# Performance work log

Hardware: AMD Instinct MI355X
Metric: run time of the kernel (lower is better)

Reference implementation:

```python
import jax, jax.numpy as jnp
import numpy as np

B, GS, IN_H, GCN_H, LIN_H = 65536, 7, 5, 144, 128


def _xavier(key, shape):
    fan_in, fan_out = shape[0], shape[1]
    limit = np.sqrt(6.0 / (fan_in + fan_out)).astype(np.float32)
    return jax.random.uniform(key, shape, jnp.float32, -limit, limit)


def setup_inputs() -> dict:
    key = jax.random.key(0)
    ks = jax.random.split(key, 12)
    operations = jax.random.normal(ks[0], (B, GS, IN_H), jnp.float32)
    adjacency = (jax.random.uniform(ks[1], (B, GS, GS)) < 0.3).astype(jnp.float32)
    num_vertices = jax.random.randint(ks[2], (B,), 1, 8).astype(jnp.float32)
    w1_0 = _xavier(ks[3], (IN_H, GCN_H))
    w2_0 = _xavier(ks[4], (IN_H, GCN_H))
    w1_1 = _xavier(ks[5], (GCN_H, GCN_H))
    w2_1 = _xavier(ks[6], (GCN_H, GCN_H))
    w1_2 = _xavier(ks[7], (GCN_H, GCN_H))
    w2_2 = _xavier(ks[8], (GCN_H, GCN_H))
    fc1_w = _xavier(ks[9], (LIN_H, GCN_H))  # torch Linear stores [out, in]
    fc2_w = _xavier(ks[10], (1, LIN_H))
    return {
        'operations': operations, 'adjacency': adjacency, 'num_vertices': num_vertices,
        'w1_0': w1_0, 'w2_0': w2_0, 'w1_1': w1_1, 'w2_1': w2_1,
        'w1_2': w1_2, 'w2_2': w2_2, 'fc1_w': fc1_w, 'fc2_w': fc2_w,
    }


def _row_normalize(adj):
    # divide each row by its sum (matches torch normalize_adj)
    return adj / adj.sum(axis=2, keepdims=True)


def reference(operations, adjacency, num_vertices,
              w1_0, w2_0, w1_1, w2_1, w1_2, w2_2, fc1_w, fc2_w):
    gs = adjacency.shape[1]
    eye = jnp.eye(gs, dtype=adjacency.dtype)
    adj_d = _row_normalize(adjacency + eye)  # [B, gs, gs]
    x = operations
    for w1, w2 in ((w1_0, w2_0), (w1_1, w2_1), (w1_2, w2_2)):
        norm_adj = _row_normalize(adj_d)                      # identity in value, kept faithful
        inv_norm_adj = _row_normalize(adj_d.transpose(0, 2, 1))
        o1 = jax.nn.relu(jnp.einsum('bij,bjk->bik', norm_adj, x @ w1))
        o2 = jax.nn.relu(jnp.einsum('bij,bjk->bik', inv_norm_adj, x @ w2))
        x = (o1 + o2) * 0.5  # dropout is identity at inference
    pooled = x.sum(axis=1) / num_vertices[:, None]            # [B, gcn_hidden]
    h = pooled @ fc1_w.T                                      # [B, linear_hidden]
    out = (h @ fc2_w.T).reshape(-1)                           # [B]
    return out
```

## Files before the change

### kernel.cpp

```cpp
#include <hip/hip_runtime.h>


typedef _Float16 half8   __attribute__((ext_vector_type(8)));
typedef _Float16 half4_t __attribute__((ext_vector_type(4)));
typedef float    floatx16 __attribute__((ext_vector_type(16)));

constexpr int GS = 7;
constexpr int NI = 4;
constexpr int MROWS = NI * GS;
constexpr int H = 144;
constexpr int LSTRIDE = 2 * 5 * 9 * 512;
constexpr int WT_HALFS = 3 * LSTRIDE;
constexpr int FRAGS = 3 * 90 * 64;
constexpr int XROW = 152;
constexpr int YROW = 40;

static __device__ inline half8 bc(_Float16 v) {
    half8 h = {v, v, v, v, v, v, v, v};
    return h;
}

__global__ void prep_kernel(const float* __restrict__ w10, const float* __restrict__ w20,
                            const float* __restrict__ w11, const float* __restrict__ w21,
                            const float* __restrict__ w12, const float* __restrict__ w22,
                            const float* __restrict__ fc1, const float* __restrict__ fc2,
                            _Float16* __restrict__ wt, float* __restrict__ g)
{
    if (blockIdx.x == 68) {
        const int j = threadIdx.x;
        if (j < H) {
            float s = 0.f;
            for (int o = 0; o < 128; ++o) s = fmaf(fc2[o], fc1[o * H + j], s);
            g[j] = s;
        }
        return;
    }
    const int t = blockIdx.x * 256 + threadIdx.x;
    if (t >= FRAGS) return;
    const int l    = t / (90 * 64);
    const int r    = t - l * (90 * 64);
    const int frag = r >> 6;
    const int lane = r & 63;
    const int p    = frag / 45;
    const int rem  = frag - p * 45;
    const int nt   = rem / 9;
    const int ks   = rem - nt * 9;
    const int m    = nt * 32 + (lane & 31);
    const int k0   = ks * 16 + (lane >> 5) * 8;
    const float* W = (l == 0) ? (p ? w20 : w10)
                   : (l == 1) ? (p ? w21 : w11)
                              : (p ? w22 : w12);
    const int K = (l == 0) ? 5 : H;
    half8 h = bc((_Float16)0);
    #pragma unroll
    for (int j = 0; j < 8; ++j) {
        const int k = k0 + j;
        if (m < H && k < K) h[j] = (_Float16)W[k * H + m];
    }
    *(half8*)(wt + (size_t)l * LSTRIDE + (size_t)frag * 512 + (size_t)lane * 8) = h;
}

template<int NK>
static __device__ __forceinline__ void layer_pass(const _Float16* __restrict__ wl,
        const int lane, const int wv, const int hi, const int m32, const int r0c,
        const int rot,
        _Float16 (*sX)[XROW], _Float16 (*sY1)[YROW], _Float16 (*sY2)[YROW],
        const half8 fN0, const half8 fN1, const half8 fI0, const half8 fI1)
{
    {
        floatx16 a1, a2;
        #pragma unroll
        for (int i = 0; i < 16; ++i) { a1[i] = 0.f; a2[i] = 0.f; }

        #pragma unroll
        for (int ks = 0; ks < NK; ++ks) {
            const half8 xa = *(const half8*)&sX[r0c][ks * 16 + hi * 8];
            const _Float16* fb = wl + (size_t)((wv * 9 + ks) * 512) + (size_t)lane * 8;
            const half8 B1 = *(const half8*)fb;
            const half8 B2 = *(const half8*)(fb + 45 * 512);
            a1 = __builtin_amdgcn_mfma_f32_32x32x16_f16(xa, B1, a1, 0, 0, 0);
            a2 = __builtin_amdgcn_mfma_f32_32x32x16_f16(xa, B2, a2, 0, 0, 0);
        }

        const int yb = wv * 32 + m32;
        #pragma unroll
        for (int q = 0; q < 4; ++q) {
            const int n0 = (8 * q + 4 * hi + rot) & 31;
            half4_t h1, h2;
            #pragma unroll
            for (int i = 0; i < 4; ++i) {
                h1[i] = (_Float16)a1[4 * q + i];
                h2[i] = (_Float16)a2[4 * q + i];
            }
            *(half4_t*)&sY1[yb][n0] = h1;
            *(half4_t*)&sY2[yb][n0] = h2;
        }
    }

    if (wv == 1) {
        floatx16 e1;
        #pragma unroll
        for (int i = 0; i < 16; ++i) e1[i] = 0.f;
        #pragma unroll
        for (int ks = 0; ks < NK; ++ks) {
            const half8 xa = *(const half8*)&sX[r0c][ks * 16 + hi * 8];
            const half8 E1 = *(const half8*)(wl + (size_t)((36 + ks) * 512) + (size_t)lane * 8);
            e1 = __builtin_amdgcn_mfma_f32_32x32x16_f16(xa, E1, e1, 0, 0, 0);
        }
        if (m32 < 16) {
            const int yb = 128 + m32;
            #pragma unroll
            for (int q = 0; q < 4; ++q) {
                const int n0 = (8 * q + 4 * hi + rot) & 31;
                half4_t h1;
                #pragma unroll
                for (int i = 0; i < 4; ++i) h1[i] = (_Float16)e1[4 * q + i];
                *(half4_t*)&sY1[yb][n0] = h1;
            }
        }
    }
    if (wv == 2) {
        floatx16 e2;
        #pragma unroll
        for (int i = 0; i < 16; ++i) e2[i] = 0.f;
        #pragma unroll
        for (int ks = 0; ks < NK; ++ks) {
            const half8 xa = *(const half8*)&sX[r0c][ks * 16 + hi * 8];
            const half8 E2 = *(const half8*)(wl + (size_t)((45 + 36 + ks) * 512) + (size_t)lane * 8);
            e2 = __builtin_amdgcn_mfma_f32_32x32x16_f16(xa, E2, e2, 0, 0, 0);
        }
        if (m32 < 16) {
            const int yb = 128 + m32;
            #pragma unroll
            for (int q = 0; q < 4; ++q) {
                const int n0 = (8 * q + 4 * hi + rot) & 31;
                half4_t h2;
                #pragma unroll
                for (int i = 0; i < 4; ++i) h2[i] = (_Float16)e2[4 * q + i];
                *(half4_t*)&sY2[yb][n0] = h2;
            }
        }
    }

    __syncthreads();

    {
        const int ybr = wv * 32 + m32;
        const half8 y10 = *(const half8*)&sY1[ybr][(hi * 8 + rot) & 31];
        const half8 y11 = *(const half8*)&sY1[ybr][(16 + hi * 8 + rot) & 31];
        const half8 y20 = *(const half8*)&sY2[ybr][(hi * 8 + rot) & 31];
        const half8 y21 = *(const half8*)&sY2[ybr][(16 + hi * 8 + rot) & 31];
        floatx16 m1, m2;
        #pragma unroll
        for (int i = 0; i < 16; ++i) { m1[i] = 0.f; m2[i] = 0.f; }
        m1 = __builtin_amdgcn_mfma_f32_32x32x16_f16(fN0, y10, m1, 0, 0, 0);
        m1 = __builtin_amdgcn_mfma_f32_32x32x16_f16(fN1, y11, m1, 0, 0, 0);
        m2 = __builtin_amdgcn_mfma_f32_32x32x16_f16(fI0, y20, m2, 0, 0, 0);
        m2 = __builtin_amdgcn_mfma_f32_32x32x16_f16(fI1, y21, m2, 0, 0, 0);
        const int col = wv * 32 + m32;
        #pragma unroll
        for (int q = 0; q < 4; ++q) {
            if (q < 3 || hi == 0) {
                #pragma unroll
                for (int i = 0; i < 4; ++i) {
                    const int n = i + 8 * q + 4 * hi;
                    float v1 = m1[4 * q + i]; v1 = v1 > 0.f ? v1 : 0.f;
                    float v2 = m2[4 * q + i]; v2 = v2 > 0.f ? v2 : 0.f;
                    sX[n][col] = (_Float16)(0.5f * (v1 + v2));
                }
            }
        }
    }
    if (wv == 3) {
        const int ybr = 128 + (m32 < 16 ? m32 : 15);
        const half8 y10 = *(const half8*)&sY1[ybr][(hi * 8 + rot) & 31];
        const half8 y11 = *(const half8*)&sY1[ybr][(16 + hi * 8 + rot) & 31];
        const half8 y20 = *(const half8*)&sY2[ybr][(hi * 8 + rot) & 31];
        const half8 y21 = *(const half8*)&sY2[ybr][(16 + hi * 8 + rot) & 31];
        floatx16 m1, m2;
        #pragma unroll
        for (int i = 0; i < 16; ++i) { m1[i] = 0.f; m2[i] = 0.f; }
        m1 = __builtin_amdgcn_mfma_f32_32x32x16_f16(fN0, y10, m1, 0, 0, 0);
        m1 = __builtin_amdgcn_mfma_f32_32x32x16_f16(fN1, y11, m1, 0, 0, 0);
        m2 = __builtin_amdgcn_mfma_f32_32x32x16_f16(fI0, y20, m2, 0, 0, 0);
        m2 = __builtin_amdgcn_mfma_f32_32x32x16_f16(fI1, y21, m2, 0, 0, 0);
        if (m32 < 16) {
            const int col = 128 + m32;
            #pragma unroll
            for (int q = 0; q < 4; ++q) {
                if (q < 3 || hi == 0) {
                    #pragma unroll
                    for (int i = 0; i < 4; ++i) {
                        const int n = i + 8 * q + 4 * hi;
                        float v1 = m1[4 * q + i]; v1 = v1 > 0.f ? v1 : 0.f;
                        float v2 = m2[4 * q + i]; v2 = v2 > 0.f ? v2 : 0.f;
                        sX[n][col] = (_Float16)(0.5f * (v1 + v2));
                    }
                }
            }
        }
    }

    __syncthreads();
}

__global__ __launch_bounds__(256, 4)
void gcn_mfma(const float* __restrict__ ops, const float* __restrict__ adj,
              const float* __restrict__ nv,
              const _Float16* __restrict__ wt, const float* __restrict__ gw,
              float* __restrict__ out)
{
    __shared__ __align__(16) _Float16 sX [MROWS][XROW];
    __shared__ __align__(16) _Float16 sY1[4 * 32 + 16][YROW];
    __shared__ __align__(16) _Float16 sY2[4 * 32 + 16][YROW];
    __shared__ __align__(16) _Float16 sAh[NI][2][GS][8];

    float (*adjd)[GS][GS] = (float(*)[GS][GS])&sY1[0][0];

    const int tid  = threadIdx.x;
    const int lane = tid & 63;
    const int wv   = tid >> 6;
    const int hi   = lane >> 5;
    const int m32  = lane & 31;
    const int rot  = m32 & 24;
    const int r0c  = (m32 < MROWS) ? m32 : (MROWS - 1);
    const int ibase = blockIdx.x * NI;

    if (tid < MROWS) {
        const int item = tid / GS, r = tid % GS;
        const float* orow = ops + ((size_t)(ibase + item) * GS + r) * 5;
        half8 h = bc((_Float16)0);
        h[0] = (_Float16)orow[0]; h[1] = (_Float16)orow[1]; h[2] = (_Float16)orow[2];
        h[3] = (_Float16)orow[3]; h[4] = (_Float16)orow[4];
        *(half8*)&sX[tid][0] = h;
        *(half8*)&sX[tid][8] = bc((_Float16)0);

        const float* arow = adj + ((size_t)(ibase + item) * GS + r) * GS;
        float a[GS]; float sm = 0.f;
        #pragma unroll
        for (int c = 0; c < GS; ++c) { a[c] = arow[c] + (c == r ? 1.f : 0.f); sm += a[c]; }
        const float is = 1.f / sm;
        #pragma unroll
        for (int c = 0; c < GS; ++c) {
            const float v = a[c] * is;
            adjd[item][r][c] = v;
            sAh[item][0][r][c] = (_Float16)v;
        }
        sAh[item][0][r][7] = (_Float16)0.f;
    }
    __syncthreads();
    if (tid < MROWS) {
        const int item = tid / GS, r = tid % GS;
        float v[GS]; float sm = 0.f;
        #pragma unroll
        for (int k = 0; k < GS; ++k) { v[k] = adjd[item][k][r]; sm += v[k]; }
        const float is = 1.f / sm;
        #pragma unroll
        for (int k = 0; k < GS; ++k) sAh[item][1][r][k] = (_Float16)(v[k] * is);
        sAh[item][1][r][7] = (_Float16)0.f;
    }
    __syncthreads();

    half8 fN0, fN1, fI0, fI1;
    {
        const int gA = m32 / 7;
        const int rA = m32 - gA * 7;
        #pragma unroll
        for (int s = 0; s < 2; ++s) {
            half8 fn = bc((_Float16)0), fi = bc((_Float16)0);
            #pragma unroll
            for (int j = 0; j < 8; ++j) {
                const int k  = s * 16 + hi * 8 + j;
                const int gK = k / 7;
                const int rK = k - gK * 7;
                if (m32 < MROWS && k < MROWS && gK == gA) {
                    fn[j] = sAh[gA][0][rA][rK];
                    fi[j] = sAh[gA][1][rA][rK];
                }
            }
            if (s == 0) { fN0 = fn; fI0 = fi; }
            else        { fN1 = fn; fI1 = fi; }
        }
    }

    layer_pass<1>(wt,                       lane, wv, hi, m32, r0c, rot, sX, sY1, sY2, fN0, fN1, fI0, fI1);
    layer_pass<9>(wt + (size_t)1 * LSTRIDE, lane, wv, hi, m32, r0c, rot, sX, sY1, sY2, fN0, fN1, fI0, fI1);
    layer_pass<9>(wt + (size_t)2 * LSTRIDE, lane, wv, hi, m32, r0c, rot, sX, sY1, sY2, fN0, fN1, fI0, fI1);

    if (tid < NI * 16) {
        const int item = tid >> 4, part = tid & 15;
        float s = 0.f;
        #pragma unroll
        for (int c = 0; c < 9; ++c) {
            const int j = part * 9 + c;
            const float gj = gw[j];
            #pragma unroll
            for (int i = 0; i < GS; ++i)
                s = fmaf((float)sX[item * GS + i][j], gj, s);
        }
        s += __shfl_xor(s, 1);
        s += __shfl_xor(s, 2);
        s += __shfl_xor(s, 4);
        s += __shfl_xor(s, 8);
        if (part == 0) out[ibase + item] = s / nv[ibase + item];
    }
}

extern "C" void kernel_launch(void* const* d_in, const int* in_sizes, int n_in,
                              void* d_out, int out_size, void* d_ws, size_t ws_size,
                              hipStream_t stream) {
    const float* ops = (const float*)d_in[0];
    const float* adj = (const float*)d_in[1];
    const float* nv  = (const float*)d_in[2];
    const float* w10 = (const float*)d_in[3];
    const float* w20 = (const float*)d_in[4];
    const float* w11 = (const float*)d_in[5];
    const float* w21 = (const float*)d_in[6];
    const float* w12 = (const float*)d_in[7];
    const float* w22 = (const float*)d_in[8];
    const float* fc1 = (const float*)d_in[9];
    const float* fc2 = (const float*)d_in[10];

    _Float16* wt = (_Float16*)d_ws;
    float*    g  = (float*)((char*)d_ws + (size_t)WT_HALFS * 2);

    prep_kernel<<<69, 256, 0, stream>>>(w10, w20, w11, w21, w12, w22,
                                        fc1, fc2, wt, g);
    gcn_mfma<<<65536 / NI, 256, 0, stream>>>(ops, adj, nv, wt, g, (float*)d_out);
}
```

Measured before the change: 293.1 us.

## Process two 4-item groups per block with register-cached layer weights

Each block now handles 8 graphs split into two 28-row groups. Each layer's weight fragments are loaded into registers once and reused for both groups, halving global/L2 weight traffic per graph. Adjacency MFMA fragments are precomputed into shared memory per group instead of being held in registers. The change raises register pressure (launch bounds lowered to 3 blocks per SM), adds more syncthreads per layer, and increases LDS use.

```diff
diff --git a/kernel.cpp b/kernel.cpp
--- a/kernel.cpp
+++ b/kernel.cpp
@@ -6,7 +6,9 @@
 typedef float    floatx16 __attribute__((ext_vector_type(16)));
 
 constexpr int GS = 7;
-constexpr int NI = 4;
+constexpr int NI = 8;
+constexpr int NG = 2;
+constexpr int GROWS = 28;
 constexpr int MROWS = NI * GS;
 constexpr int H = 144;
 constexpr int LSTRIDE = 2 * 5 * 9 * 512;
@@ -65,127 +67,115 @@
         const int lane, const int wv, const int hi, const int m32, const int r0c,
         const int rot,
         _Float16 (*sX)[XROW], _Float16 (*sY1)[YROW], _Float16 (*sY2)[YROW],
-        const half8 fN0, const half8 fN1, const half8 fI0, const half8 fI1)
+        const _Float16 (*sAf)[64 * 8])
 {
-    {
-        floatx16 a1, a2;
-        #pragma unroll
-        for (int i = 0; i < 16; ++i) { a1[i] = 0.f; a2[i] = 0.f; }
-
-        #pragma unroll
-        for (int ks = 0; ks < NK; ++ks) {
-            const half8 xa = *(const half8*)&sX[r0c][ks * 16 + hi * 8];
-            const _Float16* fb = wl + (size_t)((wv * 9 + ks) * 512) + (size_t)lane * 8;
-            const half8 B1 = *(const half8*)fb;
-            const half8 B2 = *(const half8*)(fb + 45 * 512);
-            a1 = __builtin_amdgcn_mfma_f32_32x32x16_f16(xa, B1, a1, 0, 0, 0);
-            a2 = __builtin_amdgcn_mfma_f32_32x32x16_f16(xa, B2, a2, 0, 0, 0);
-        }
-
-        const int yb = wv * 32 + m32;
-        #pragma unroll
-        for (int q = 0; q < 4; ++q) {
-            const int n0 = (8 * q + 4 * hi + rot) & 31;
-            half4_t h1, h2;
-            #pragma unroll
-            for (int i = 0; i < 4; ++i) {
-                h1[i] = (_Float16)a1[4 * q + i];
-                h2[i] = (_Float16)a2[4 * q + i];
-            }
-            *(half4_t*)&sY1[yb][n0] = h1;
-            *(half4_t*)&sY2[yb][n0] = h2;
-        }
-    }
-
-    if (wv == 1) {
-        floatx16 e1;
-        #pragma unroll
-        for (int i = 0; i < 16; ++i) e1[i] = 0.f;
-        #pragma unroll
-        for (int ks = 0; ks < NK; ++ks) {
-            const half8 xa = *(const half8*)&sX[r0c][ks * 16 + hi * 8];
-            const half8 E1 = *(const half8*)(wl + (size_t)((36 + ks) * 512) + (size_t)lane * 8);
-            e1 = __builtin_amdgcn_mfma_f32_32x32x16_f16(xa, E1, e1, 0, 0, 0);
-        }
-        if (m32 < 16) {
-            const int yb = 128 + m32;
+    half8 wA[NK], wB[NK];
+    #pragma unroll
+    for (int ks = 0; ks < NK; ++ks) {
+        const _Float16* fb = wl + (size_t)((wv * 9 + ks) * 512) + (size_t)lane * 8;
+        wA[ks] = *(const half8*)fb;
+        wB[ks] = *(const half8*)(fb + 45 * 512);
+    }
+    half8 eT[NK];
+    if (wv == 1 || wv == 2) {
+        const int poff = (wv == 2) ? 45 * 512 : 0;
+        #pragma unroll
+        for (int ks = 0; ks < NK; ++ks)
+            eT[ks] = *(const half8*)(wl + (size_t)((36 + ks) * 512) + poff + (size_t)lane * 8);
+    }
+
+    #pragma unroll
+    for (int g = 0; g < NG; ++g) {
+        const int rbase = g * GROWS;
+
+        {
+            floatx16 a1, a2;
+            #pragma unroll
+            for (int i = 0; i < 16; ++i) { a1[i] = 0.f; a2[i] = 0.f; }
+            #pragma unroll
+            for (int ks = 0; ks < NK; ++ks) {
+                const half8 xa = *(const half8*)&sX[rbase + r0c][ks * 16 + hi * 8];
+                a1 = __builtin_amdgcn_mfma_f32_32x32x16_f16(xa, wA[ks], a1, 0, 0, 0);
+                a2 = __builtin_amdgcn_mfma_f32_32x32x16_f16(xa, wB[ks], a2, 0, 0, 0);
+            }
+            const int yb = wv * 32 + m32;
             #pragma unroll
             for (int q = 0; q < 4; ++q) {
                 const int n0 = (8 * q + 4 * hi + rot) & 31;
-                half4_t h1;
-                #pragma unroll
-                for (int i = 0; i < 4; ++i) h1[i] = (_Float16)e1[4 * q + i];
-                *(half4_t*)&sY1[yb][n0] = h1;
-            }
-        }
-    }
-    if (wv == 2) {
-        floatx16 e2;
-        #pragma unroll
-        for (int i = 0; i < 16; ++i) e2[i] = 0.f;
-        #pragma unroll
-        for (int ks = 0; ks < NK; ++ks) {
-            const half8 xa = *(const half8*)&sX[r0c][ks * 16 + hi * 8];
-            const half8 E2 = *(const half8*)(wl + (size_t)((45 + 36 + ks) * 512) + (size_t)lane * 8);
-            e2 = __builtin_amdgcn_mfma_f32_32x32x16_f16(xa, E2, e2, 0, 0, 0);
-        }
-        if (m32 < 16) {
-            const int yb = 128 + m32;
-            #pragma unroll
-            for (int q = 0; q < 4; ++q) {
-                const int n0 = (8 * q + 4 * hi + rot) & 31;
-                half4_t h2;
-                #pragma unroll
-                for (int i = 0; i < 4; ++i) h2[i] = (_Float16)e2[4 * q + i];
-                *(half4_t*)&sY2[yb][n0] = h2;
-            }
-        }
-    }
-
-    __syncthreads();
-
-    {
-        const int ybr = wv * 32 + m32;
-        const half8 y10 = *(const half8*)&sY1[ybr][(hi * 8 + rot) & 31];
-        const half8 y11 = *(const half8*)&sY1[ybr][(16 + hi * 8 + rot) & 31];
-        const half8 y20 = *(const half8*)&sY2[ybr][(hi * 8 + rot) & 31];
-        const half8 y21 = *(const half8*)&sY2[ybr][(16 + hi * 8 + rot) & 31];
-        floatx16 m1, m2;
-        #pragma unroll
-        for (int i = 0; i < 16; ++i) { m1[i] = 0.f; m2[i] = 0.f; }
-        m1 = __builtin_amdgcn_mfma_f32_32x32x16_f16(fN0, y10, m1, 0, 0, 0);
-        m1 = __builtin_amdgcn_mfma_f32_32x32x16_f16(fN1, y11, m1, 0, 0, 0);
-        m2 = __builtin_amdgcn_mfma_f32_32x32x16_f16(fI0, y20, m2, 0, 0, 0);
-        m2 = __builtin_amdgcn_mfma_f32_32x32x16_f16(fI1, y21, m2, 0, 0, 0);
-        const int col = wv * 32 + m32;
-        #pragma unroll
-        for (int q = 0; q < 4; ++q) {
-            if (q < 3 || hi == 0) {
+                half4_t h1, h2;
                 #pragma unroll
                 for (int i = 0; i < 4; ++i) {
-                    const int n = i + 8 * q + 4 * hi;
-                    float v1 = m1[4 * q + i]; v1 = v1 > 0.f ? v1 : 0.f;
-                    float v2 = m2[4 * q + i]; v2 = v2 > 0.f ? v2 : 0.f;
-                    sX[n][col] = (_Float16)(0.5f * (v1 + v2));
-                }
-            }
-        }
-    }
-    if (wv == 3) {
-        const int ybr = 128 + (m32 < 16 ? m32 : 15);
-        const half8 y10 = *(const half8*)&sY1[ybr][(hi * 8 + rot) & 31];
-        const half8 y11 = *(const half8*)&sY1[ybr][(16 + hi * 8 + rot) & 31];
-        const half8 y20 = *(const half8*)&sY2[ybr][(hi * 8 + rot) & 31];
-        const half8 y21 = *(const half8*)&sY2[ybr][(16 + hi * 8 + rot) & 31];
-        floatx16 m1, m2;
-        #pragma unroll
-        for (int i = 0; i < 16; ++i) { m1[i] = 0.f; m2[i] = 0.f; }
-        m1 = __builtin_amdgcn_mfma_f32_32x32x16_f16(fN0, y10, m1, 0, 0, 0);
-        m1 = __builtin_amdgcn_mfma_f32_32x32x16_f16(fN1, y11, m1, 0, 0, 0);
-        m2 = __builtin_amdgcn_mfma_f32_32x32x16_f16(fI0, y20, m2, 0, 0, 0);
-        m2 = __builtin_amdgcn_mfma_f32_32x32x16_f16(fI1, y21, m2, 0, 0, 0);
-        if (m32 < 16) {
-            const int col = 128 + m32;
+                    h1[i] = (_Float16)a1[4 * q + i];
+                    h2[i] = (_Float16)a2[4 * q + i];
+                }
+                *(half4_t*)&sY1[yb][n0] = h1;
+                *(half4_t*)&sY2[yb][n0] = h2;
+            }
+        }
+
+        if (wv == 1) {
+            floatx16 e1;
+            #pragma unroll
+            for (int i = 0; i < 16; ++i) e1[i] = 0.f;
+            #pragma unroll
+            for (int ks = 0; ks < NK; ++ks) {
+                const half8 xa = *(const half8*)&sX[rbase + r0c][ks * 16 + hi * 8];
+                e1 = __builtin_amdgcn_mfma_f32_32x32x16_f16(xa, eT[ks], e1, 0, 0, 0);
+            }
+            if (m32 < 16) {
+                const int yb = 128 + m32;
+                #pragma unroll
+                for (int q = 0; q < 4; ++q) {
+                    const int n0 = (8 * q + 4 * hi + rot) & 31;
+                    half4_t h1;
+                    #pragma unroll
+                    for (int i = 0; i < 4; ++i) h1[i] = (_Float16)e1[4 * q + i];
+                    *(half4_t*)&sY1[yb][n0] = h1;
+                }
+            }
+        }
+        if (wv == 2) {
+            floatx16 e2;
+            #pragma unroll
+            for (int i = 0; i < 16; ++i) e2[i] = 0.f;
+            #pragma unroll
+            for (int ks = 0; ks < NK; ++ks) {
+                const half8 xa = *(const half8*)&sX[rbase + r0c][ks * 16 + hi * 8];
+                e2 = __builtin_amdgcn_mfma_f32_32x32x16_f16(xa, eT[ks], e2, 0, 0, 0);
+            }
+            if (m32 < 16) {
+                const int yb = 128 + m32;
+                #pragma unroll
+                for (int q = 0; q < 4; ++q) {
+                    const int n0 = (8 * q + 4 * hi + rot) & 31;
+                    half4_t h2;
+                    #pragma unroll
+                    for (int i = 0; i < 4; ++i) h2[i] = (_Float16)e2[4 * q + i];
+                    *(half4_t*)&sY2[yb][n0] = h2;
+                }
+            }
+        }
+
+        __syncthreads();
+
+        {
+            const half8 fN0 = *(const half8*)&sAf[(g * 2 + 0) * 2 + 0][lane * 8];
+            const half8 fN1 = *(const half8*)&sAf[(g * 2 + 0) * 2 + 1][lane * 8];
+            const half8 fI0 = *(const half8*)&sAf[(g * 2 + 1) * 2 + 0][lane * 8];
+            const half8 fI1 = *(const half8*)&sAf[(g * 2 + 1) * 2 + 1][lane * 8];
+            const int ybr = wv * 32 + m32;
+            const half8 y10 = *(const half8*)&sY1[ybr][(hi * 8 + rot) & 31];
+            const half8 y11 = *(const half8*)&sY1[ybr][(16 + hi * 8 + rot) & 31];
+            const half8 y20 = *(const half8*)&sY2[ybr][(hi * 8 + rot) & 31];
+            const half8 y21 = *(const half8*)&sY2[ybr][(16 + hi * 8 + rot) & 31];
+            floatx16 m1, m2;
+            #pragma unroll
+            for (int i = 0; i < 16; ++i) { m1[i] = 0.f; m2[i] = 0.f; }
+            m1 = __builtin_amdgcn_mfma_f32_32x32x16_f16(fN0, y10, m1, 0, 0, 0);
+            m1 = __builtin_amdgcn_mfma_f32_32x32x16_f16(fN1, y11, m1, 0, 0, 0);
+            m2 = __builtin_amdgcn_mfma_f32_32x32x16_f16(fI0, y20, m2, 0, 0, 0);
+            m2 = __builtin_amdgcn_mfma_f32_32x32x16_f16(fI1, y21, m2, 0, 0, 0);
+            const int col = wv * 32 + m32;
             #pragma unroll
             for (int q = 0; q < 4; ++q) {
                 if (q < 3 || hi == 0) {
@@ -194,26 +184,60 @@
                         const int n = i + 8 * q + 4 * hi;
                         float v1 = m1[4 * q + i]; v1 = v1 > 0.f ? v1 : 0.f;
                         float v2 = m2[4 * q + i]; v2 = v2 > 0.f ? v2 : 0.f;
-                        sX[n][col] = (_Float16)(0.5f * (v1 + v2));
+                        sX[rbase + n][col] = (_Float16)(0.5f * (v1 + v2));
                     }
                 }
             }
         }
-    }
-
-    __syncthreads();
-}
-
-__global__ __launch_bounds__(256, 4)
+        if (wv == 3) {
+            const half8 fN0 = *(const half8*)&sAf[(g * 2 + 0) * 2 + 0][lane * 8];
+            const half8 fN1 = *(const half8*)&sAf[(g * 2 + 0) * 2 + 1][lane * 8];
+            const half8 fI0 = *(const half8*)&sAf[(g * 2 + 1) * 2 + 0][lane * 8];
+            const half8 fI1 = *(const half8*)&sAf[(g * 2 + 1) * 2 + 1][lane * 8];
+            const int ybr = 128 + (m32 < 16 ? m32 : 15);
+            const half8 y10 = *(const half8*)&sY1[ybr][(hi * 8 + rot) & 31];
+            const half8 y11 = *(const half8*)&sY1[ybr][(16 + hi * 8 + rot) & 31];
+            const half8 y20 = *(const half8*)&sY2[ybr][(hi * 8 + rot) & 31];
+            const half8 y21 = *(const half8*)&sY2[ybr][(16 + hi * 8 + rot) & 31];
+            floatx16 m1, m2;
+            #pragma unroll
+            for (int i = 0; i < 16; ++i) { m1[i] = 0.f; m2[i] = 0.f; }
+            m1 = __builtin_amdgcn_mfma_f32_32x32x16_f16(fN0, y10, m1, 0, 0, 0);
+            m1 = __builtin_amdgcn_mfma_f32_32x32x16_f16(fN1, y11, m1, 0, 0, 0);
+            m2 = __builtin_amdgcn_mfma_f32_32x32x16_f16(fI0, y20, m2, 0, 0, 0);
+            m2 = __builtin_amdgcn_mfma_f32_32x32x16_f16(fI1, y21, m2, 0, 0, 0);
+            if (m32 < 16) {
+                const int col = 128 + m32;
+                #pragma unroll
+                for (int q = 0; q < 4; ++q) {
+                    if (q < 3 || hi == 0) {
+                        #pragma unroll
+                        for (int i = 0; i < 4; ++i) {
+                            const int n = i + 8 * q + 4 * hi;
+                            float v1 = m1[4 * q + i]; v1 = v1 > 0.f ? v1 : 0.f;
+                            float v2 = m2[4 * q + i]; v2 = v2 > 0.f ? v2 : 0.f;
+                            sX[rbase + n][col] = (_Float16)(0.5f * (v1 + v2));
+                        }
+                    }
+                }
+            }
+        }
+
+        __syncthreads();
+    }
+}
+
+__global__ __launch_bounds__(256, 3)
 void gcn_mfma(const float* __restrict__ ops, const float* __restrict__ adj,
               const float* __restrict__ nv,
               const _Float16* __restrict__ wt, const float* __restrict__ gw,
               float* __restrict__ out)
 {
     __shared__ __align__(16) _Float16 sX [MROWS][XROW];
-    __shared__ __align__(16) _Float16 sY1[4 * 32 + 16][YROW];
-    __shared__ __align__(16) _Float16 sY2[4 * 32 + 16][YROW];
+    __shared__ __align__(16) _Float16 sY1[4 * 32 + 32][YROW];
+    __shared__ __align__(16) _Float16 sY2[4 * 32 + 32][YROW];
     __shared__ __align__(16) _Float16 sAh[NI][2][GS][8];
+    __shared__ __align__(16) _Float16 sAf[8][64 * 8];
 
     float (*adjd)[GS][GS] = (float(*)[GS][GS])&sY1[0][0];
 
@@ -223,7 +247,7 @@
     const int hi   = lane >> 5;
     const int m32  = lane & 31;
     const int rot  = m32 & 24;
-    const int r0c  = (m32 < MROWS) ? m32 : (MROWS - 1);
+    const int r0c  = (m32 < GROWS) ? m32 : (GROWS - 1);
     const int ibase = blockIdx.x * NI;
 
     if (tid < MROWS) {
@@ -261,31 +285,27 @@
     }
     __syncthreads();
 
-    half8 fN0, fN1, fI0, fI1;
-    {
-        const int gA = m32 / 7;
-        const int rA = m32 - gA * 7;
-        #pragma unroll
-        for (int s = 0; s < 2; ++s) {
-            half8 fn = bc((_Float16)0), fi = bc((_Float16)0);
-            #pragma unroll
-            for (int j = 0; j < 8; ++j) {
-                const int k  = s * 16 + hi * 8 + j;
-                const int gK = k / 7;
-                const int rK = k - gK * 7;
-                if (m32 < MROWS && k < MROWS && gK == gA) {
-                    fn[j] = sAh[gA][0][rA][rK];
-                    fi[j] = sAh[gA][1][rA][rK];
-                }
-            }
-            if (s == 0) { fN0 = fn; fI0 = fi; }
-            else        { fN1 = fn; fI1 = fi; }
-        }
-    }
-
-    layer_pass<1>(wt,                       lane, wv, hi, m32, r0c, rot, sX, sY1, sY2, fN0, fN1, fI0, fI1);
-    layer_pass<9>(wt + (size_t)1 * LSTRIDE, lane, wv, hi, m32, r0c, rot, sX, sY1, sY2, fN0, fN1, fI0, fI1);
-    layer_pass<9>(wt + (size_t)2 * LSTRIDE, lane, wv, hi, m32, r0c, rot, sX, sY1, sY2, fN0, fN1, fI0, fI1);
+    #pragma unroll
+    for (int rep = 0; rep < 2; ++rep) {
+        const int e  = tid + rep * 256;
+        const int gg = e >> 8, pp = (e >> 7) & 1, ss = (e >> 6) & 1, ll = e & 63;
+        const int hh = ll >> 5, nn = ll & 31;
+        const int gA = nn / 7, rA = nn - 7 * gA;
+        half8 f = bc((_Float16)0);
+        #pragma unroll
+        for (int j = 0; j < 8; ++j) {
+            const int k  = ss * 16 + hh * 8 + j;
+            const int gK = k / 7, rK = k - 7 * gK;
+            if (nn < GROWS && k < GROWS && gK == gA)
+                f[j] = sAh[gg * 4 + gA][pp][rA][rK];
+        }
+        *(half8*)&sAf[(gg * 2 + pp) * 2 + ss][ll * 8] = f;
+    }
+    __syncthreads();
+
+    layer_pass<1>(wt,                       lane, wv, hi, m32, r0c, rot, sX, sY1, sY2, sAf);
+    layer_pass<9>(wt + (size_t)1 * LSTRIDE, lane, wv, hi, m32, r0c, rot, sX, sY1, sY2, sAf);
+    layer_pass<9>(wt + (size_t)2 * LSTRIDE, lane, wv, hi, m32, r0c, rot, sX, sY1, sY2, sAf);
 
     if (tid < NI * 16) {
         const int item = tid >> 4, part = tid & 15;
```

New measurement: 444.4 us. +51.6%, slower.
